# Kernel optimization log

Measured on AMD Instinct MI355X. Metric: run time of the kernel, lower is better.

Reference implementation:

```python
import jax, jax.numpy as jnp
import numpy as np

Q_HEADS, KV_HEADS, DIMS, IN_DIMS = 16, 4, 1024, 1024
HEAD_D = DIMS // Q_HEADS            # 64
GROUPS = Q_HEADS // KV_HEADS        # 4
ROPE_BASE = 10000.0


def nd_rope(x, coords):
    """N-D rotary embedding.
    x: [..., s, d]; coords: broadcastable [..., s, a] (float).
    Head dim d is split into a contiguous chunks of d//a; within each chunk
    consecutive pairs (2i, 2i+1) are rotated by angle coord_axis * base^(-2i/(d//a)).
    """
    a = coords.shape[-1]
    d = x.shape[-1]
    dpa = d // a                                  # dims per coordinate axis (even)
    inv_freq = ROPE_BASE ** (-jnp.arange(dpa // 2, dtype=jnp.float32) * (2.0 / dpa))
    angles = coords[..., :, None] * inv_freq      # [..., s, a, dpa//2]
    angles = angles.reshape(angles.shape[:-2] + (d // 2,))
    cos, sin = jnp.cos(angles), jnp.sin(angles)
    xp = x.reshape(x.shape[:-1] + (d // 2, 2))
    x1, x2 = xp[..., 0], xp[..., 1]
    return jnp.stack([x1 * cos - x2 * sin, x1 * sin + x2 * cos], axis=-1).reshape(x.shape)


def setup_inputs() -> dict:
    key = jax.random.key(0)
    k1, k2, k3, k4, k5, k6, k7, k8 = jax.random.split(key, 8)
    B, SQ, SKV, A = 4, 2048, 2048, 2
    q = jax.random.normal(k1, (B, SQ, IN_DIMS), dtype=jnp.float32)
    kv = jax.random.normal(k2, (B, SKV, IN_DIMS), dtype=jnp.float32)
    q_coords = jax.random.randint(k3, (B, SQ, A), 0, 2048, dtype=jnp.int32)
    kv_coords = jax.random.randint(k4, (B, SKV, A), 0, 2048, dtype=jnp.int32)
    s_in = 1.0 / np.sqrt(IN_DIMS)
    Wq = jax.random.normal(k5, (IN_DIMS, Q_HEADS, HEAD_D), dtype=jnp.float32) * s_in
    Wk = jax.random.normal(k6, (IN_DIMS, KV_HEADS, HEAD_D), dtype=jnp.float32) * s_in
    Wv = jax.random.normal(k7, (IN_DIMS, KV_HEADS, HEAD_D), dtype=jnp.float32) * s_in
    Wo = jax.random.normal(k8, (KV_HEADS * HEAD_D, IN_DIMS), dtype=jnp.float32) * (1.0 / np.sqrt(KV_HEADS * HEAD_D))
    return {"q": q, "q_coords": q_coords, "kv": kv, "kv_coords": kv_coords,
            "Wq": Wq, "Wk": Wk, "Wv": Wv, "Wo": Wo}


def reference(q, q_coords, kv, kv_coords, Wq, Wk, Wv, Wo):
    B, SQ = q.shape[0], q.shape[1]
    qp = jnp.einsum('bsi,ihd->bshd', q, Wq)   # [b, sq, q_heads, hd]
    kp = jnp.einsum('bsi,ihd->bshd', kv, Wk)  # [b, skv, kv_heads, hd]
    vp = jnp.einsum('bsi,ihd->bshd', kv, Wv)
    # '... s (h g) d -> ... g h s d' with h=KV_HEADS outer, g=GROUPS inner
    qp = qp.reshape(B, SQ, KV_HEADS, GROUPS, HEAD_D).transpose(0, 3, 2, 1, 4)  # [b,g,h,sq,hd]
    kp = kp.transpose(0, 2, 1, 3)  # [b,h,skv,hd]
    vp = vp.transpose(0, 2, 1, 3)
    qc = q_coords.astype(jnp.float32)[:, None, None]  # [b,1,1,sq,a] -> broadcast over g,h
    kc = kv_coords.astype(jnp.float32)[:, None]       # [b,1,skv,a] -> broadcast over h
    qr = nd_rope(qp, qc)
    kr = nd_rope(kp, kc)
    # NOTE: einops pattern omits g in output -> group axis is SUMMED (faithful to source)
    scores = jnp.einsum('bghsd,bhad->bhsa', qr, kr) / (HEAD_D ** 0.5)
    attn = jax.nn.softmax(scores, axis=-1)
    out = jnp.einsum('bhsa,bhad->bhsd', attn, vp)
    out = out.transpose(0, 2, 1, 3).reshape(B, SQ, KV_HEADS * HEAD_D)
    return out @ Wo
```

## Files before the change

### kernel.cpp

```cpp
#include <hip/hip_runtime.h>

#define BATCH 4
#define SEQQ  2048
#define SEQKV 2048
#define NH    4
#define HD    64
#define IND   1024
#define QSCL 0.18033688011112042f

typedef __attribute__((ext_vector_type(8))) short short8;
typedef __attribute__((ext_vector_type(4))) short s4v;
typedef __attribute__((ext_vector_type(4))) float floatx4;

#if defined(__HIP_DEVICE_COMPILE__) && __has_builtin(__builtin_amdgcn_exp2f)
  #define EXP2(x) __builtin_amdgcn_exp2f(x)
#else
  #define EXP2(x) exp2f(x)
#endif

#if defined(__HIP_DEVICE_COMPILE__)
  #if __has_builtin(__builtin_amdgcn_mfma_f32_16x16x16bf16_1k)
    #define MFMA16(a, b, c) __builtin_amdgcn_mfma_f32_16x16x16bf16_1k(a, b, c, 0, 0, 0)
  #elif __has_builtin(__builtin_amdgcn_mfma_f32_16x16x16_bf16)
    #define MFMA16(a, b, c) __builtin_amdgcn_mfma_f32_16x16x16_bf16(a, b, c, 0, 0, 0)
  #else
    #error "no 16x16x16 bf16 MFMA builtin on gfx950 device pass"
  #endif
#else
  #define MFMA16(a, b, c) (c)
#endif
#define MFMA32(a, b, c) __builtin_amdgcn_mfma_f32_16x16x32_bf16(a, b, c, 0, 0, 0)

__device__ __forceinline__ short f2b(float f) {
    unsigned u; __builtin_memcpy(&u, &f, 4);
    u = (u + 0x7fffu + ((u >> 16) & 1u)) >> 16;
    return (short)u;
}
__device__ __forceinline__ short8 cvt8(const float* p) {
    float4 a = *(const float4*)p;
    float4 b = *(const float4*)(p + 4);
    short8 r;
    r[0] = f2b(a.x); r[1] = f2b(a.y); r[2] = f2b(a.z); r[3] = f2b(a.w);
    r[4] = f2b(b.x); r[5] = f2b(b.y); r[6] = f2b(b.z); r[7] = f2b(b.w);
    return r;
}

__global__ __launch_bounds__(256) void prep_all(
    const float* __restrict__ Wq, const float* __restrict__ Wk,
    const float* __restrict__ Wv, const float* __restrict__ Wo,
    const float* __restrict__ q, const float* __restrict__ kv,
    short* __restrict__ Wq_t, short* __restrict__ Wkv_t, short* __restrict__ Wo_t,
    short* __restrict__ qb, short* __restrict__ kvb) {
    __shared__ short Ts[64][65];
    int blk = blockIdx.x;
    if (blk < 256) {
        int c4 = threadIdx.x & 63, r4 = threadIdx.x >> 6;
        if (blk < 64) {
            int h = blk & 3, ib = blk >> 2;
#pragma unroll 4
            for (int jj = 0; jj < 16; ++jj) {
                int il = r4 * 16 + jj;
                float s = 0.f;
#pragma unroll
                for (int g = 0; g < 4; ++g)
                    s += Wq[(ib * 64 + il) * 1024 + (h * 4 + g) * 64 + c4];
                Ts[il][c4] = f2b(s);
            }
            __syncthreads();
#pragma unroll 4
            for (int jj = 0; jj < 16; ++jj) {
                int dl = r4 * 16 + jj;
                Wq_t[(h * 64 + dl) * 1024 + ib * 64 + c4] = Ts[c4][dl];
            }
        } else if (blk < 192) {
            int t = blk - 64, ss = t >> 6; t &= 63;
            int ib = t >> 2, nb = t & 3;
            const float* W = ss ? Wv : Wk;
#pragma unroll 4
            for (int jj = 0; jj < 16; ++jj) {
                int il = r4 * 16 + jj;
                Ts[il][c4] = f2b(W[(ib * 64 + il) * 256 + nb * 64 + c4]);
            }
            __syncthreads();
#pragma unroll 4
            for (int jj = 0; jj < 16; ++jj) {
                int dl = r4 * 16 + jj;
                Wkv_t[(ss * 256 + nb * 64 + dl) * 1024 + ib * 64 + c4] = Ts[c4][dl];
            }
        } else {
            int t = blk - 192, kb = t >> 4, nb = t & 15;
#pragma unroll 4
            for (int jj = 0; jj < 16; ++jj) {
                int il = r4 * 16 + jj;
                Ts[il][c4] = f2b(Wo[(kb * 64 + il) * 1024 + nb * 64 + c4]);
            }
            __syncthreads();
#pragma unroll 4
            for (int jj = 0; jj < 16; ++jj) {
                int dl = r4 * 16 + jj;
                Wo_t[(nb * 64 + dl) * 256 + kb * 64 + c4] = Ts[c4][dl];
            }
        }
    } else if (blk < 4352) {
        long e = ((long)(blk - 256) * 256 + threadIdx.x) * 8;
        *(short8*)(qb + e) = cvt8(q + e);
    } else {
        long e = ((long)(blk - 4352) * 256 + threadIdx.x) * 8;
        *(short8*)(kvb + e) = cvt8(kv + e);
    }
}

template <int MODE>
__device__ __forceinline__ void gemm128(
    const short* __restrict__ A, const short* __restrict__ Wt,
    int m0, int n0, int N, int K, short* As, short* Bs,
    float* __restrict__ C, const int* __restrict__ coords,
    short* __restrict__ ropeDst, short* __restrict__ vDst) {
    const int t = threadIdx.x;
    const int w = t >> 6, lane = t & 63, ln = lane & 15, quad = lane >> 4;
    const int wm = w >> 1, wn = w & 1;
    const int srow = lane >> 2, skc = (lane & 3) * 8;
    floatx4 acc[4][4];
#pragma unroll
    for (int mt = 0; mt < 4; ++mt)
#pragma unroll
        for (int nt = 0; nt < 4; ++nt) acc[mt][nt] = floatx4{0.f, 0.f, 0.f, 0.f};

    for (int ks = 0; ks < K; ks += 32) {
        __syncthreads();
#pragma unroll
        for (int i = 0; i < 2; ++i) {
            __builtin_amdgcn_global_load_lds(
                (const void*)(A + (long)(m0 + w * 32 + i * 16 + srow) * K + ks + skc),
                (void*)(As + (w * 2 + i) * 512), 16, 0, 0);
            __builtin_amdgcn_global_load_lds(
                (const void*)(Wt + (long)(n0 + w * 32 + i * 16 + srow) * K + ks + skc),
                (void*)(Bs + (w * 2 + i) * 512), 16, 0, 0);
        }
        __syncthreads();
        short8 af[4], bf[4];
#pragma unroll
        for (int mt = 0; mt < 4; ++mt)
            af[mt] = *(const short8*)(As + (wm * 64 + mt * 16 + ln) * 32 + quad * 8);
#pragma unroll
        for (int nt = 0; nt < 4; ++nt)
            bf[nt] = *(const short8*)(Bs + (wn * 64 + nt * 16 + ln) * 32 + quad * 8);
#pragma unroll
        for (int mt = 0; mt < 4; ++mt)
#pragma unroll
            for (int nt = 0; nt < 4; ++nt)
                acc[mt][nt] = MFMA32(af[mt], bf[nt], acc[mt][nt]);
    }

    if (MODE == 0) {
#pragma unroll
        for (int mt = 0; mt < 4; ++mt) {
            int row0 = m0 + wm * 64 + mt * 16 + quad * 4;
#pragma unroll
            for (int nt = 0; nt < 4; ++nt) {
                int col = n0 + wn * 64 + nt * 16 + ln;
#pragma unroll
                for (int r = 0; r < 4; ++r)
                    C[(long)(row0 + r) * N + col] = acc[mt][nt][r];
            }
        }
    } else {
        const int wn_col = n0 + wn * 64;
        if (MODE == 1 || wn_col < 256) {
            const int h = (wn_col >> 6) & 3;
            const float scl = (MODE == 1) ? QSCL : 1.0f;
            const float L = -0.5756462732485114f;
            const float fA = __expf((float)(ln >> 1) * L);
            const float fB = __expf((float)(8 + (ln >> 1)) * L);
            const float sgn = (ln & 1) ? 1.0f : -1.0f;
#pragma unroll
            for (int mt = 0; mt < 4; ++mt) {
                int row0 = m0 + wm * 64 + mt * 16 + quad * 4;
#pragma unroll
                for (int r = 0; r < 4; ++r) {
                    int row = row0 + r;
                    float c0 = (float)coords[row * 2];
                    float c1 = (float)coords[row * 2 + 1];
                    float snv[4], csv[4];
                    __sincosf(c0 * fA, &snv[0], &csv[0]);
                    __sincosf(c0 * fB, &snv[1], &csv[1]);
                    __sincosf(c1 * fA, &snv[2], &csv[2]);
                    __sincosf(c1 * fB, &snv[3], &csv[3]);
                    long rbase = ((long)((row >> 11) * 4 + h) * 2048 + (row & 2047)) * 64;
#pragma unroll
                    for (int nt = 0; nt < 4; ++nt) {
                        float v = acc[mt][nt][r];
                        float p = __shfl_xor(v, 1, 64);
                        float o = v * (csv[nt] * scl) + p * (snv[nt] * (scl * sgn));
                        ropeDst[rbase + nt * 16 + ln] = f2b(o);
                    }
                }
            }
        } else {
            const int h = ((wn_col - 256) >> 6) & 3;
#pragma unroll
            for (int mt = 0; mt < 4; ++mt) {
                int row0 = m0 + wm * 64 + mt * 16 + quad * 4;
                int b = row0 >> 11, s0 = row0 & 2047;
#pragma unroll
                for (int nt = 0; nt < 4; ++nt) {
                    s4v ov;
#pragma unroll
                    for (int r = 0; r < 4; ++r) ov[r] = f2b(acc[mt][nt][r]);
                    *(s4v*)(vDst + (long)((b * 4 + h) * 64 + nt * 16 + ln) * 2048 + s0) = ov;
                }
            }
        }
    }
}

__global__ __launch_bounds__(256) void proj_gemm(
    const short* __restrict__ qb, const short* __restrict__ kvb,
    const short* __restrict__ Wq_t, const short* __restrict__ Wkv_t,
    const int* __restrict__ qc, const int* __restrict__ kvc,
    short* __restrict__ Qr, short* __restrict__ Kr, short* __restrict__ Vt) {
    __shared__ __align__(16) short As[128 * 32];
    __shared__ __align__(16) short Bs[128 * 32];
    int id = blockIdx.x;
    if (id < 128)
        gemm128<1>(qb, Wq_t, (id >> 1) * 128, (id & 1) * 128, 256, 1024, As, Bs,
                   nullptr, qc, Qr, nullptr);
    else {
        int t = id - 128;
        gemm128<2>(kvb, Wkv_t, (t >> 2) * 128, (t & 3) * 128, 512, 1024, As, Bs,
                   nullptr, kvc, Kr, Vt);
    }
}

__global__ __launch_bounds__(256) void final_gemm(
    const short* __restrict__ Ob, const short* __restrict__ Wo_t, float* __restrict__ out) {
    __shared__ __align__(16) short As[128 * 32];
    __shared__ __align__(16) short Bs[128 * 32];
    gemm128<0>(Ob, Wo_t, blockIdx.x * 128, blockIdx.y * 128, 1024, 256, As, Bs,
               out, nullptr, nullptr, nullptr);
}

__global__ __launch_bounds__(256, 4) void attn_kernel(
    const short* __restrict__ Qr, const short* __restrict__ Kr,
    const short* __restrict__ Vt, float* __restrict__ Op, float* __restrict__ Lp) {
    __shared__ __align__(16) short Kls[64 * 64];
    __shared__ __align__(16) short Vls[64 * 64];
    const int blk = blockIdx.x;
    const int bh = blk & 15, sp = (blk >> 4) & 3, qg = blk >> 6;
    const int w = threadIdx.x >> 6, lane = threadIdx.x & 63;
    const int ln = lane & 15, quad = lane >> 4;
    const int q0 = qg * 128 + w * 32;
    const short* Qb = Qr + (long)bh * SEQKV * HD;
    const short* Kb = Kr + (long)bh * SEQKV * HD;
    const short* Vb = Vt + (long)bh * HD * SEQKV;

    const int srow = lane >> 3;
    const int schk = (lane & 7) ^ (srow & 7);
    const long kstage0 = (long)(w * 16 + srow) * HD + schk * 8;
    const long vstage0 = (long)(w * 16 + srow) * SEQKV + schk * 8;

    short8 qf[2][2];
#pragma unroll
    for (int qs = 0; qs < 2; ++qs)
#pragma unroll
        for (int ck = 0; ck < 2; ++ck)
            qf[qs][ck] = *(const short8*)(Qb + (long)(q0 + qs * 16 + ln) * HD + ck * 32 + quad * 8);

    s4v ones;
#pragma unroll
    for (int j = 0; j < 4; ++j) ones[j] = (short)0x3F80;

    floatx4 o[2][4], ol[2];
#pragma unroll
    for (int qs = 0; qs < 2; ++qs) {
        ol[qs] = floatx4{0.f, 0.f, 0.f, 0.f};
#pragma unroll
        for (int nt = 0; nt < 4; ++nt) o[qs][nt] = floatx4{0.f, 0.f, 0.f, 0.f};
    }

    const int ln7 = ln & 7;
    int koff[2];
#pragma unroll
    for (int ck = 0; ck < 2; ++ck) koff[ck] = ln * 64 + ((ck * 4 + quad) ^ ln7) * 8;
    int voff[4];
#pragma unroll
    for (int t = 0; t < 4; ++t) voff[t] = ln * 64 + ((t * 2 + (quad >> 1)) ^ ln7) * 8 + (quad & 1) * 4;

    for (int kt = sp * 512; kt < sp * 512 + 512; kt += 64) {
        __syncthreads();
#pragma unroll
        for (int i = 0; i < 2; ++i) {
            __builtin_amdgcn_global_load_lds(
                (const void*)(Kb + (long)kt * HD + kstage0 + (long)i * 8 * HD),
                (void*)(Kls + (w * 16 + i * 8) * 64), 16, 0, 0);
            __builtin_amdgcn_global_load_lds(
                (const void*)(Vb + kt + vstage0 + (long)i * 8 * SEQKV),
                (void*)(Vls + (w * 16 + i * 8) * 64), 16, 0, 0);
        }
        __syncthreads();

#pragma unroll
        for (int t = 0; t < 4; ++t) {
            short8 a0 = *(const short8*)(Kls + t * 1024 + koff[0]);
            short8 a1 = *(const short8*)(Kls + t * 1024 + koff[1]);
            floatx4 st0 = {0.f, 0.f, 0.f, 0.f}, st1 = {0.f, 0.f, 0.f, 0.f};
            st0 = MFMA32(a0, qf[0][0], st0);
            st1 = MFMA32(a0, qf[1][0], st1);
            st0 = MFMA32(a1, qf[0][1], st0);
            st1 = MFMA32(a1, qf[1][1], st1);
            s4v pt0, pt1;
#pragma unroll
            for (int j = 0; j < 4; ++j) {
                float p0 = EXP2(st0[j]);
                float p1 = EXP2(st1[j]);
                unsigned u0, u1;
                __builtin_memcpy(&u0, &p0, 4); __builtin_memcpy(&u1, &p1, 4);
                pt0[j] = (short)((u0 + 0x8000u) >> 16);
                pt1[j] = (short)((u1 + 0x8000u) >> 16);
            }
#pragma unroll
            for (int nt = 0; nt < 4; ++nt) {
                s4v vf = *(const s4v*)(Vls + nt * 1024 + voff[t]);
                o[0][nt] = MFMA16(vf, pt0, o[0][nt]);
                o[1][nt] = MFMA16(vf, pt1, o[1][nt]);
            }
            ol[0] = MFMA16(ones, pt0, ol[0]);
            ol[1] = MFMA16(ones, pt1, ol[1]);
        }
    }
#pragma unroll
    for (int qs = 0; qs < 2; ++qs) {
        long qrow = (long)(sp * 16 + bh) * 2048 + q0 + qs * 16 + ln;
        if (quad == 0) Lp[qrow] = ol[qs][0];
#pragma unroll
        for (int nt = 0; nt < 4; ++nt)
            *(floatx4*)(Op + qrow * 64 + nt * 16 + quad * 4) = o[qs][nt];
    }
}

__global__ __launch_bounds__(256) void combine_kernel(
    const float* __restrict__ Op, const float* __restrict__ Lp, short* __restrict__ Ob) {
    int row = blockIdx.x * 4 + (threadIdx.x >> 6);
    int d = threadIdx.x & 63;
    int bh = row >> 11, qq = row & 2047;
    int b = bh >> 2, h = bh & 3;
    float os = 0.f, ls = 0.f;
#pragma unroll
    for (int s = 0; s < 4; ++s) {
        long rr = (long)(s * 16 + bh) * 2048 + qq;
        os += Op[rr * 64 + d];
        ls += Lp[rr];
    }
    Ob[((long)(b * 2048 + qq)) * 256 + h * 64 + d] = f2b(os / ls);
}

extern "C" void kernel_launch(void* const* d_in, const int* in_sizes, int n_in,
                              void* d_out, int out_size, void* d_ws, size_t ws_size,
                              hipStream_t stream) {
    const float* q   = (const float*)d_in[0];
    const int*   qc  = (const int*)d_in[1];
    const float* kv  = (const float*)d_in[2];
    const int*   kvc = (const int*)d_in[3];
    const float* Wq  = (const float*)d_in[4];
    const float* Wk  = (const float*)d_in[5];
    const float* Wv  = (const float*)d_in[6];
    const float* Wo  = (const float*)d_in[7];
    float* out = (float*)d_out;

    char* ws = (char*)d_ws;
    const size_t MB = 1024 * 1024;
    short* Wq_t  = (short*)(ws);
    short* Wkv_t = (short*)(ws + MB / 2);
    short* Wo_t  = (short*)(ws + 3 * MB / 2);
    short* qb    = (short*)(ws + 2 * MB);
    short* kvb   = (short*)(ws + 18 * MB);
    short* Qr    = (short*)(ws + 34 * MB);
    short* Kr    = (short*)(ws + 38 * MB);
    short* Vt    = (short*)(ws + 42 * MB);
    short* Ob    = (short*)(ws + 46 * MB);
    float* Opart = (float*)(ws + 50 * MB);
    float* Lpart = (float*)(ws + 82 * MB);

    hipLaunchKernelGGL(prep_all, dim3(8448), dim3(256), 0, stream,
                       Wq, Wk, Wv, Wo, q, kv, Wq_t, Wkv_t, Wo_t, qb, kvb);
    hipLaunchKernelGGL(proj_gemm, dim3(384), dim3(256), 0, stream,
                       qb, kvb, Wq_t, Wkv_t, qc, kvc, Qr, Kr, Vt);
    hipLaunchKernelGGL(attn_kernel, dim3(1024), dim3(256), 0, stream,
                       Qr, Kr, Vt, Opart, Lpart);
    hipLaunchKernelGGL(combine_kernel, dim3(8192), dim3(256), 0, stream,
                       Opart, Lpart, Ob);
    hipLaunchKernelGGL(final_gemm, dim3(64, 8), dim3(256), 0, stream, Ob, Wo_t, out);
}
```

Baseline: 193.1 us.

## Double-buffer attention K/V staging and vectorize prep and combine kernels

The attention kernel now uses two LDS buffers for K and V, so the next 64-key tile is prefetched while the current one is computed, with one barrier per iteration instead of two. The prep conversion kernel handles 16 elements per thread with half as many blocks. The combine kernel reads float4 and writes four bf16 values per thread. Together these aim to hide load latency and cut per-thread overhead, at the cost of doubled LDS use in attention, which may lower occupancy.

```diff
diff --git a/kernel.cpp b/kernel.cpp
--- a/kernel.cpp
+++ b/kernel.cpp
@@ -101,12 +101,14 @@
                 Wo_t[(nb * 64 + dl) * 256 + kb * 64 + c4] = Ts[c4][dl];
             }
         }
-    } else if (blk < 4352) {
-        long e = ((long)(blk - 256) * 256 + threadIdx.x) * 8;
-        *(short8*)(qb + e) = cvt8(q + e);
+    } else if (blk < 2304) {
+        long e = ((long)(blk - 256) * 256 + threadIdx.x) * 16;
+        *(short8*)(qb + e)     = cvt8(q + e);
+        *(short8*)(qb + e + 8) = cvt8(q + e + 8);
     } else {
-        long e = ((long)(blk - 4352) * 256 + threadIdx.x) * 8;
-        *(short8*)(kvb + e) = cvt8(kv + e);
+        long e = ((long)(blk - 2304) * 256 + threadIdx.x) * 16;
+        *(short8*)(kvb + e)     = cvt8(kv + e);
+        *(short8*)(kvb + e + 8) = cvt8(kv + e + 8);
     }
 }
 
@@ -243,8 +245,8 @@
 __global__ __launch_bounds__(256, 4) void attn_kernel(
     const short* __restrict__ Qr, const short* __restrict__ Kr,
     const short* __restrict__ Vt, float* __restrict__ Op, float* __restrict__ Lp) {
-    __shared__ __align__(16) short Kls[64 * 64];
-    __shared__ __align__(16) short Vls[64 * 64];
+    __shared__ __align__(16) short Kls[2][64 * 64];
+    __shared__ __align__(16) short Vls[2][64 * 64];
     const int blk = blockIdx.x;
     const int bh = blk & 15, sp = (blk >> 4) & 3, qg = blk >> 6;
     const int w = threadIdx.x >> 6, lane = threadIdx.x & 63;
@@ -286,23 +288,31 @@
 #pragma unroll
     for (int t = 0; t < 4; ++t) voff[t] = ln * 64 + ((t * 2 + (quad >> 1)) ^ ln7) * 8 + (quad & 1) * 4;
 
-    for (int kt = sp * 512; kt < sp * 512 + 512; kt += 64) {
-        __syncthreads();
-#pragma unroll
-        for (int i = 0; i < 2; ++i) {
-            __builtin_amdgcn_global_load_lds(
-                (const void*)(Kb + (long)kt * HD + kstage0 + (long)i * 8 * HD),
-                (void*)(Kls + (w * 16 + i * 8) * 64), 16, 0, 0);
-            __builtin_amdgcn_global_load_lds(
-                (const void*)(Vb + kt + vstage0 + (long)i * 8 * SEQKV),
-                (void*)(Vls + (w * 16 + i * 8) * 64), 16, 0, 0);
-        }
-        __syncthreads();
-
+    const int kt0 = sp * 512;
+#define STAGE(kt, sel)                                                              \
+    do {                                                                            \
+        _Pragma("unroll")                                                           \
+        for (int i = 0; i < 2; ++i) {                                               \
+            __builtin_amdgcn_global_load_lds(                                       \
+                (const void*)(Kb + (long)(kt) * HD + kstage0 + (long)i * 8 * HD),   \
+                (void*)(Kls[sel] + (w * 16 + i * 8) * 64), 16, 0, 0);               \
+            __builtin_amdgcn_global_load_lds(                                       \
+                (const void*)(Vb + (kt) + vstage0 + (long)i * 8 * SEQKV),           \
+                (void*)(Vls[sel] + (w * 16 + i * 8) * 64), 16, 0, 0);               \
+        }                                                                           \
+    } while (0)
+
+    STAGE(kt0, 0);
+    __syncthreads();
+    int cur = 0;
+    for (int tt = 0; tt < 8; ++tt) {
+        if (tt < 7) STAGE(kt0 + (tt + 1) * 64, cur ^ 1);
+        const short* Kc = Kls[cur];
+        const short* Vc = Vls[cur];
 #pragma unroll
         for (int t = 0; t < 4; ++t) {
-            short8 a0 = *(const short8*)(Kls + t * 1024 + koff[0]);
-            short8 a1 = *(const short8*)(Kls + t * 1024 + koff[1]);
+            short8 a0 = *(const short8*)(Kc + t * 1024 + koff[0]);
+            short8 a1 = *(const short8*)(Kc + t * 1024 + koff[1]);
             floatx4 st0 = {0.f, 0.f, 0.f, 0.f}, st1 = {0.f, 0.f, 0.f, 0.f};
             st0 = MFMA32(a0, qf[0][0], st0);
             st1 = MFMA32(a0, qf[1][0], st1);
@@ -320,14 +330,17 @@
             }
 #pragma unroll
             for (int nt = 0; nt < 4; ++nt) {
-                s4v vf = *(const s4v*)(Vls + nt * 1024 + voff[t]);
+                s4v vf = *(const s4v*)(Vc + nt * 1024 + voff[t]);
                 o[0][nt] = MFMA16(vf, pt0, o[0][nt]);
                 o[1][nt] = MFMA16(vf, pt1, o[1][nt]);
             }
             ol[0] = MFMA16(ones, pt0, ol[0]);
             ol[1] = MFMA16(ones, pt1, ol[1]);
         }
-    }
+        __syncthreads();
+        cur ^= 1;
+    }
+#undef STAGE
 #pragma unroll
     for (int qs = 0; qs < 2; ++qs) {
         long qrow = (long)(sp * 16 + bh) * 2048 + q0 + qs * 16 + ln;
@@ -340,18 +353,25 @@
 
 __global__ __launch_bounds__(256) void combine_kernel(
     const float* __restrict__ Op, const float* __restrict__ Lp, short* __restrict__ Ob) {
-    int row = blockIdx.x * 4 + (threadIdx.x >> 6);
-    int d = threadIdx.x & 63;
+    int idx = blockIdx.x * 256 + threadIdx.x;
+    int row = idx >> 4;
+    int d0 = (idx & 15) * 4;
     int bh = row >> 11, qq = row & 2047;
     int b = bh >> 2, h = bh & 3;
-    float os = 0.f, ls = 0.f;
+    float4 os = {0.f, 0.f, 0.f, 0.f};
+    float ls = 0.f;
 #pragma unroll
     for (int s = 0; s < 4; ++s) {
         long rr = (long)(s * 16 + bh) * 2048 + qq;
-        os += Op[rr * 64 + d];
+        float4 v = *(const float4*)(Op + rr * 64 + d0);
+        os.x += v.x; os.y += v.y; os.z += v.z; os.w += v.w;
         ls += Lp[rr];
     }
-    Ob[((long)(b * 2048 + qq)) * 256 + h * 64 + d] = f2b(os / ls);
+    float li = 1.f / ls;
+    s4v ov;
+    ov[0] = f2b(os.x * li); ov[1] = f2b(os.y * li);
+    ov[2] = f2b(os.z * li); ov[3] = f2b(os.w * li);
+    *(s4v*)(Ob + ((long)(b * 2048 + qq)) * 256 + h * 64 + d0) = ov;
 }
 
 extern "C" void kernel_launch(void* const* d_in, const int* in_sizes, int n_in,
@@ -381,13 +401,13 @@
     float* Opart = (float*)(ws + 50 * MB);
     float* Lpart = (float*)(ws + 82 * MB);
 
-    hipLaunchKernelGGL(prep_all, dim3(8448), dim3(256), 0, stream,
+    hipLaunchKernelGGL(prep_all, dim3(4352), dim3(256), 0, stream,
                        Wq, Wk, Wv, Wo, q, kv, Wq_t, Wkv_t, Wo_t, qb, kvb);
     hipLaunchKernelGGL(proj_gemm, dim3(384), dim3(256), 0, stream,
                        qb, kvb, Wq_t, Wkv_t, qc, kvc, Qr, Kr, Vt);
     hipLaunchKernelGGL(attn_kernel, dim3(1024), dim3(256), 0, stream,
                        Qr, Kr, Vt, Opart, Lpart);
-    hipLaunchKernelGGL(combine_kernel, dim3(8192), dim3(256), 0, stream,
+    hipLaunchKernelGGL(combine_kernel, dim3(2048), dim3(256), 0, stream,
                        Opart, Lpart, Ob);
     hipLaunchKernelGGL(final_gemm, dim3(64, 8), dim3(256), 0, stream, Ob, Wo_t, out);
 }
```

Result: no change. 191.3 us (-0.9%).
